# Kernel optimization log

Hardware: AMD Instinct MI355X
Metric: run time of the kernel (lower is better)

The kernel has to match this reference:

```python
import jax, jax.numpy as jnp
import numpy as np

# Static configuration (matches init_kwargs)
B, S = 1, 2048          # batch, stacked seq len
IN, D, OUT = 64, 1024, 128
H, HD = 16, 64          # heads, head_dim (rope over full head_dim)
L, FFN = 4, 4096        # layers, SwiGLU hidden
WIN = 128               # encoder_sliding_window
DOC = 256               # each of the 8 stacked documents has length 256
THETA = 10000.0
EPS = 1e-5


def setup_inputs() -> dict:
    key = jax.random.key(0)
    ks = jax.random.split(key, 12)
    std = 0.02  # init_base_std
    p = lambda k, shp: jax.random.normal(k, shp, jnp.float32) * std
    idx = jnp.arange(S, dtype=jnp.int32)
    return {
        "x": jax.random.normal(ks[0], (B, S, IN), jnp.float32),
        "emb_w": p(ks[1], (IN, D)),
        "emb_b": jnp.zeros((D,), jnp.float32),
        "wq": p(ks[2], (L, D, H * HD)),
        "wk": p(ks[3], (L, D, H * HD)),
        "wv": p(ks[4], (L, D, H * HD)),
        "wo": p(ks[5], (L, H * HD, D)),
        "attn_norm_w": jnp.ones((L, D), jnp.float32),
        "ffn_norm_w": jnp.ones((L, D), jnp.float32),
        "w1": p(ks[6], (L, D, FFN)),
        "w2": p(ks[7], (L, FFN, D)),
        "w3": p(ks[8], (L, D, FFN)),
        "out_norm_w": jnp.ones((D,), jnp.float32),
        "out_w": p(ks[9], (D, OUT)),
        "doc_id": idx // DOC,   # sequence-stacked document ids
        "tok_id": idx % DOC,    # per-document local token ids
    }


def _rmsnorm(x, w):
    return x * jax.lax.rsqrt(jnp.mean(x * x, axis=-1, keepdims=True) + EPS) * w


def _rope_cos_sin(tok_id):
    inv = 1.0 / (THETA ** (jnp.arange(0, HD, 2, dtype=jnp.float32) / HD))  # [HD/2]
    ang = tok_id.astype(jnp.float32)[:, None] * inv[None, :]               # [S, HD/2]
    return jnp.cos(ang), jnp.sin(ang)


def _apply_rope(x, cos, sin):
    # x: [B, S, H, HD]; rotate-half convention over head_dim
    x1, x2 = jnp.split(x, 2, axis=-1)
    c = cos[None, :, None, :]
    s = sin[None, :, None, :]
    return jnp.concatenate([x1 * c - x2 * s, x1 * s + x2 * c], axis=-1)


def reference(x, emb_w, emb_b, wq, wk, wv, wo, attn_norm_w, ffn_norm_w,
              w1, w2, w3, out_norm_w, out_w, doc_id, tok_id):
    # doc + sliding-window mask (the flex_attention mask_mod): same document
    same_doc = doc_id[:, None] == doc_id[None, :]
    t = tok_id.astype(jnp.int32)
    in_win = jnp.abs(t[:, None] - t[None, :]) < WIN
    mask = same_doc & in_win                       # [S, S] bool
    neg = jnp.asarray(jnp.finfo(jnp.float32).min, jnp.float32)

    cos, sin = _rope_cos_sin(tok_id)
    scale = 1.0 / np.sqrt(HD)

    h = x @ emb_w + emb_b                          # tok_embeddings: [B, S, D]

    def layer(h, p):
        wq_l, wk_l, wv_l, wo_l, anw, fnw, w1_l, w2_l, w3_l = p
        hn = _rmsnorm(h, anw)
        q = _apply_rope((hn @ wq_l).reshape(B, S, H, HD), cos, sin)
        k = _apply_rope((hn @ wk_l).reshape(B, S, H, HD), cos, sin)
        v = (hn @ wv_l).reshape(B, S, H, HD)
        scores = jnp.einsum("bqhd,bkhd->bhqk", q, k) * scale
        scores = jnp.where(mask[None, None], scores, neg)
        probs = jax.nn.softmax(scores, axis=-1)
        o = jnp.einsum("bhqk,bkhd->bqhd", probs, v).reshape(B, S, H * HD)
        h = h + o @ wo_l
        hn2 = _rmsnorm(h, fnw)
        ffn = (jax.nn.silu(hn2 @ w1_l) * (hn2 @ w3_l)) @ w2_l  # SwiGLU
        return h + ffn, None

    h, _ = jax.lax.scan(layer, h, (wq, wk, wv, wo, attn_norm_w, ffn_norm_w, w1, w2, w3))
    return _rmsnorm(h, out_norm_w) @ out_w         # output proj: [B, S, OUT]
```

## Files before the change

### kernel.cpp

```cpp
#include <hip/hip_runtime.h>
#include <hip/hip_bf16.h>

typedef __attribute__((ext_vector_type(8))) short short8;
typedef __attribute__((ext_vector_type(4))) float float4v;

__device__ __forceinline__ float bf2f(ushort u) {
    union { unsigned int i; float f; } x; x.i = ((unsigned int)u) << 16; return x.f;
}
__device__ __forceinline__ ushort f2bf(float f) {
    union { float f; unsigned int i; } x; x.f = f;
    unsigned int i = x.i;
    unsigned int r = (i + 0x7fffu + ((i >> 16) & 1u)) >> 16;
    return (ushort)r;
}

__global__ __launch_bounds__(256) void transpose4_f2b(const float* __restrict__ s0,
                                                      const float* __restrict__ s1,
                                                      const float* __restrict__ s2,
                                                      const float* __restrict__ s3,
                                                      ushort* __restrict__ dst,
                                                      int K, int N) {
    __shared__ ushort tile[64][68];
    const float* srcs[4] = {s0, s1, s2, s3};
    const float* src = srcs[blockIdx.z];
    ushort* d = dst + (size_t)blockIdx.z * K * N;
    const int t = threadIdx.x;
    const int n0 = blockIdx.x * 64, k0 = blockIdx.y * 64;
    const int tr = t >> 4, tc = (t & 15) * 4;
#pragma unroll
    for (int i = 0; i < 4; ++i) {
        int row = tr + i * 16;
        float4 v = *(const float4*)&src[(size_t)(k0 + row) * N + n0 + tc];
        tile[row][tc + 0] = f2bf(v.x);
        tile[row][tc + 1] = f2bf(v.y);
        tile[row][tc + 2] = f2bf(v.z);
        tile[row][tc + 3] = f2bf(v.w);
    }
    __syncthreads();
#pragma unroll
    for (int i = 0; i < 4; ++i) {
        int n = tr + i * 16;
        ushort4 v;
        v.x = tile[tc + 0][n]; v.y = tile[tc + 1][n];
        v.z = tile[tc + 2][n]; v.w = tile[tc + 3][n];
        *(ushort4*)&d[(size_t)(n0 + n) * K + k0 + tc] = v;
    }
}

__global__ __launch_bounds__(256) void embed_k(const float* __restrict__ x,
                                               const float* __restrict__ w,
                                               const float* __restrict__ b,
                                               float* __restrict__ h) {
    const int row = blockIdx.y;
    const int col = blockIdx.x * 256 + threadIdx.x;
    float acc = b[col];
#pragma unroll 8
    for (int k = 0; k < 64; ++k)
        acc += x[row * 64 + k] * w[k * 1024 + col];
    h[(size_t)row * 1024 + col] = acc;
}

__global__ __launch_bounds__(256) void rmsnorm_k(const float* __restrict__ h,
                                                 const float* __restrict__ w,
                                                 ushort* __restrict__ out) {
    const int row = blockIdx.x, t = threadIdx.x;
    float4 v = ((const float4*)(h + (size_t)row * 1024))[t];
    float ss = v.x * v.x + v.y * v.y + v.z * v.z + v.w * v.w;
#pragma unroll
    for (int off = 32; off > 0; off >>= 1) ss += __shfl_down(ss, off);
    __shared__ float red[4];
    if ((t & 63) == 0) red[t >> 6] = ss;
    __syncthreads();
    float inv = rsqrtf((red[0] + red[1] + red[2] + red[3]) * (1.0f / 1024.0f) + 1e-5f);
    float4 wv = ((const float4*)w)[t];
    ushort4 ov;
    ov.x = f2bf(v.x * inv * wv.x);
    ov.y = f2bf(v.y * inv * wv.y);
    ov.z = f2bf(v.z * inv * wv.z);
    ov.w = f2bf(v.w * inv * wv.w);
    *(ushort4*)&out[(size_t)row * 1024 + t * 4] = ov;
}

__global__ __launch_bounds__(256) void rope_table_k(float* __restrict__ ct,
                                                    float* __restrict__ st) {
    int idx = blockIdx.x * 256 + threadIdx.x;
    int s = idx >> 5, j = idx & 31;
    float inv = expf(-(float)j * (1.0f / 32.0f) * logf(10000.0f));
    float ang = (float)(s & 255) * inv;
    ct[idx] = cosf(ang);
    st[idx] = sinf(ang);
}

__global__ __launch_bounds__(256) void rope_apply_k(ushort* __restrict__ qkv,
                                                    const float* __restrict__ ct,
                                                    const float* __restrict__ st) {
    int idx = blockIdx.x * 256 + threadIdx.x;
    int j = idx & 31;
    int head = (idx >> 5) & 15;
    int s = idx >> 9;
    size_t base = (size_t)s * 3072 + head * 64 + j;
    float c = ct[s * 32 + j], sn = st[s * 32 + j];
    float x1 = bf2f(qkv[base]), x2 = bf2f(qkv[base + 32]);
    qkv[base] = f2bf(x1 * c - x2 * sn);
    qkv[base + 32] = f2bf(x1 * sn + x2 * c);
    x1 = bf2f(qkv[base + 1024]); x2 = bf2f(qkv[base + 1056]);
    qkv[base + 1024] = f2bf(x1 * c - x2 * sn);
    qkv[base + 1056] = f2bf(x1 * sn + x2 * c);
}

__global__ __launch_bounds__(256) void silu_mul_k(ushort* __restrict__ t13) {
    int idx = blockIdx.x * 256 + threadIdx.x;
    int s = idx >> 10, c4 = (idx & 1023) * 4;
    size_t b1 = (size_t)s * 8192 + c4;
    ushort4 a = *(ushort4*)&t13[b1];
    ushort4 b = *(ushort4*)&t13[b1 + 4096];
    float xs[4] = {bf2f(a.x), bf2f(a.y), bf2f(a.z), bf2f(a.w)};
    float ys[4] = {bf2f(b.x), bf2f(b.y), bf2f(b.z), bf2f(b.w)};
    ushort4 o;
    o.x = f2bf(xs[0] / (1.0f + __expf(-xs[0])) * ys[0]);
    o.y = f2bf(xs[1] / (1.0f + __expf(-xs[1])) * ys[1]);
    o.z = f2bf(xs[2] / (1.0f + __expf(-xs[2])) * ys[2]);
    o.w = f2bf(xs[3] / (1.0f + __expf(-xs[3])) * ys[3]);
    *(ushort4*)&t13[b1] = o;
}

__global__ __launch_bounds__(256) void reduce4_k(const ushort* __restrict__ p,
                                                 float* __restrict__ h,
                                                 int ldp, long zstr, int cbase) {
    const int s = blockIdx.x, c = threadIdx.x * 4;
    size_t base = (size_t)s * ldp + cbase + c;
    float a0 = 0, a1 = 0, a2 = 0, a3 = 0;
#pragma unroll
    for (int z = 0; z < 4; ++z) {
        ushort4 v = *(const ushort4*)&p[base + (size_t)z * zstr];
        a0 += bf2f(v.x); a1 += bf2f(v.y); a2 += bf2f(v.z); a3 += bf2f(v.w);
    }
    float4* hp = (float4*)&h[(size_t)s * 1024 + c];
    float4 cur = *hp;
    cur.x += a0; cur.y += a1; cur.z += a2; cur.w += a3;
    *hp = cur;
}

template <int OUT, int SK>
__global__ __launch_bounds__(256) void gemm_bt(const ushort* __restrict__ A, int lda,
                                               const ushort* __restrict__ Bt,
                                               void* __restrict__ Cp,
                                               int N, int K,
                                               int ldc, long zstr, int cbase) {
    __shared__ ushort As[128 * 32];
    __shared__ ushort Bs[128 * 32];
    const int tid = threadIdx.x, wave = tid >> 6, lane = tid & 63;
    const int quad = lane >> 4, l15 = lane & 15;
    const int m0 = blockIdx.y * 128, n0 = blockIdx.x * 128;
    const int wm = wave & 1, wn = wave >> 1;
    const int Kc = K / SK;
    const int kbeg = blockIdx.z * Kc, kend = kbeg + Kc;
    float4v acc[4][4] = {};
    for (int k0 = kbeg; k0 < kend; k0 += 32) {
        __syncthreads();
#pragma unroll
        for (int h = 0; h < 2; ++h) {
            int c = wave * 2 + h;
            int mrow = c * 16 + (lane >> 2);
            int kb = (lane & 3) * 16;
            const char* ga = (const char*)A + ((size_t)(m0 + mrow) * lda + k0) * 2 + kb;
            __builtin_amdgcn_global_load_lds(
                (const __attribute__((address_space(1))) void*)ga,
                (__attribute__((address_space(3))) void*)((char*)As + c * 1024), 16, 0, 0);
            const char* gb = (const char*)Bt + ((size_t)(n0 + mrow) * K + k0) * 2 + kb;
            __builtin_amdgcn_global_load_lds(
                (const __attribute__((address_space(1))) void*)gb,
                (__attribute__((address_space(3))) void*)((char*)Bs + c * 1024), 16, 0, 0);
        }
        __syncthreads();
        short8 af[4], bf[4];
#pragma unroll
        for (int i = 0; i < 4; ++i)
            af[i] = *(const short8*)((const char*)As + (wm * 64 + i * 16 + l15) * 64 + quad * 16);
#pragma unroll
        for (int j = 0; j < 4; ++j)
            bf[j] = *(const short8*)((const char*)Bs + (wn * 64 + j * 16 + l15) * 64 + quad * 16);
#pragma unroll
        for (int i = 0; i < 4; ++i)
#pragma unroll
            for (int j = 0; j < 4; ++j)
                acc[i][j] = __builtin_amdgcn_mfma_f32_16x16x32_bf16(af[i], bf[j], acc[i][j], 0, 0, 0);
    }
    const size_t zoff = (OUT == 3) ? (size_t)cbase + (size_t)blockIdx.z * zstr : 0;
#pragma unroll
    for (int i = 0; i < 4; ++i)
#pragma unroll
        for (int j = 0; j < 4; ++j)
#pragma unroll
            for (int r = 0; r < 4; ++r) {
                int row = m0 + wm * 64 + i * 16 + quad * 4 + r;
                int col = n0 + wn * 64 + j * 16 + l15;
                if (OUT == 0) {
                    ((ushort*)Cp)[(size_t)row * ldc + col] = f2bf(acc[i][j][r]);
                } else if (OUT == 2) {
                    ((float*)Cp)[(size_t)row * ldc + col] = acc[i][j][r];
                } else {
                    ((ushort*)Cp)[zoff + (size_t)row * ldc + col] = f2bf(acc[i][j][r]);
                }
            }
}

__global__ __launch_bounds__(512) void attention_k(const ushort* __restrict__ qkv,
                                                   ushort* __restrict__ o) {
    __shared__ ushort Vt[64 * 264];
    __shared__ ushort Pc[8][16 * 40];
    const int tid = threadIdx.x, wave = tid >> 6, lane = tid & 63;
    const int quad = lane >> 4, l15 = lane & 15;
    const int doc = blockIdx.x >> 5, head = (blockIdx.x >> 1) & 15, qh = blockIdx.x & 1;
    const size_t S0 = (size_t)doc * 256;

    const ushort* vb = qkv + 2048 + head * 64;
    for (int i = tid; i < 256 * 64; i += 512) {
        int key = i >> 6, d = i & 63;
        Vt[d * 264 + key] = vb[(S0 + key) * 3072 + d];
    }

    const int q0 = qh * 128 + wave * 16;
    const ushort* qbase = qkv + head * 64;
    const ushort* kbase = qkv + 1024 + head * 64;
    short8 af0 = *(const short8*)&qbase[(S0 + q0 + l15) * 3072 + quad * 8];
    short8 af1 = *(const short8*)&qbase[(S0 + q0 + l15) * 3072 + 32 + quad * 8];

    float4v acc[16];
#pragma unroll
    for (int nt = 0; nt < 16; ++nt) {
        short8 b0 = *(const short8*)&kbase[(S0 + nt * 16 + l15) * 3072 + quad * 8];
        short8 b1 = *(const short8*)&kbase[(S0 + nt * 16 + l15) * 3072 + 32 + quad * 8];
        float4v a = {0.0f, 0.0f, 0.0f, 0.0f};
        a = __builtin_amdgcn_mfma_f32_16x16x32_bf16(af0, b0, a, 0, 0, 0);
        a = __builtin_amdgcn_mfma_f32_16x16x32_bf16(af1, b1, a, 0, 0, 0);
        acc[nt] = a;
    }

    float mx[4] = {-1e30f, -1e30f, -1e30f, -1e30f};
#pragma unroll
    for (int nt = 0; nt < 16; ++nt)
#pragma unroll
        for (int r = 0; r < 4; ++r) {
            int qp = q0 + quad * 4 + r;
            int kp = nt * 16 + l15;
            int dlt = qp - kp;
            bool ok = (dlt < 128) && (dlt > -128);
            float s = ok ? acc[nt][r] * 0.125f : -1e30f;
            acc[nt][r] = s;
            mx[r] = fmaxf(mx[r], s);
        }
#pragma unroll
    for (int r = 0; r < 4; ++r) {
        mx[r] = fmaxf(mx[r], __shfl_xor(mx[r], 1));
        mx[r] = fmaxf(mx[r], __shfl_xor(mx[r], 2));
        mx[r] = fmaxf(mx[r], __shfl_xor(mx[r], 4));
        mx[r] = fmaxf(mx[r], __shfl_xor(mx[r], 8));
    }
    float sum[4] = {0.0f, 0.0f, 0.0f, 0.0f};
#pragma unroll
    for (int nt = 0; nt < 16; ++nt)
#pragma unroll
        for (int r = 0; r < 4; ++r) {
            float p = __expf(acc[nt][r] - mx[r]);
            acc[nt][r] = p;
            sum[r] += p;
        }
    float inv[4];
#pragma unroll
    for (int r = 0; r < 4; ++r) {
        sum[r] += __shfl_xor(sum[r], 1);
        sum[r] += __shfl_xor(sum[r], 2);
        sum[r] += __shfl_xor(sum[r], 4);
        sum[r] += __shfl_xor(sum[r], 8);
        inv[r] = 1.0f / sum[r];
    }

    __syncthreads();

    float4v oacc[4] = {};
    ushort* pcw = &Pc[wave][0];
#pragma unroll
    for (int ks = 0; ks < 8; ++ks) {
#pragma unroll
        for (int half = 0; half < 2; ++half) {
            int nt = ks * 2 + half;
#pragma unroll
            for (int r = 0; r < 4; ++r)
                pcw[(quad * 4 + r) * 40 + half * 16 + l15] = f2bf(acc[nt][r] * inv[r]);
        }
        __asm__ volatile("s_waitcnt lgkmcnt(0)" ::: "memory");
        short8 pf = *(const short8*)&pcw[l15 * 40 + quad * 8];
#pragma unroll
        for (int ntd = 0; ntd < 4; ++ntd) {
            short8 vf = *(const short8*)&Vt[(ntd * 16 + l15) * 264 + ks * 32 + quad * 8];
            oacc[ntd] = __builtin_amdgcn_mfma_f32_16x16x32_bf16(pf, vf, oacc[ntd], 0, 0, 0);
        }
    }
#pragma unroll
    for (int ntd = 0; ntd < 4; ++ntd)
#pragma unroll
        for (int r = 0; r < 4; ++r)
            o[(S0 + q0 + quad * 4 + r) * 1024 + head * 64 + ntd * 16 + l15] = f2bf(oacc[ntd][r]);
}

extern "C" void kernel_launch(void* const* d_in, const int* in_sizes, int n_in,
                              void* d_out, int out_size, void* d_ws, size_t ws_size,
                              hipStream_t stream) {
    const float* x     = (const float*)d_in[0];
    const float* emb_w = (const float*)d_in[1];
    const float* emb_b = (const float*)d_in[2];
    const float* wq    = (const float*)d_in[3];
    const float* wk    = (const float*)d_in[4];
    const float* wv    = (const float*)d_in[5];
    const float* wo    = (const float*)d_in[6];
    const float* anw   = (const float*)d_in[7];
    const float* fnw   = (const float*)d_in[8];
    const float* w1    = (const float*)d_in[9];
    const float* w2    = (const float*)d_in[10];
    const float* w3    = (const float*)d_in[11];
    const float* onw   = (const float*)d_in[12];
    const float* ow    = (const float*)d_in[13];

    char* ws = (char*)d_ws;
    float*  h    = (float*)(ws);
    ushort* hn   = (ushort*)(ws + (8u << 20));
    ushort* big  = (ushort*)(ws + (12u << 20));
    ushort* pwo  = (ushort*)(ws + (24u << 20));
    ushort* wbuf = (ushort*)(ws + (44u << 20));
    float*  cosT = (float*)(ws + (60u << 20));
    float*  sinT = (float*)(ws + (60u << 20) + (256u << 10));

    dim3 b256(256);
    rope_table_k<<<256, b256, 0, stream>>>(cosT, sinT);
    embed_k<<<dim3(4, 2048), b256, 0, stream>>>(x, emb_w, emb_b, h);

    for (int l = 0; l < 4; ++l) {
        const float* wq_l = wq + (size_t)l * 1024 * 1024;
        const float* wk_l = wk + (size_t)l * 1024 * 1024;
        const float* wv_l = wv + (size_t)l * 1024 * 1024;
        const float* wo_l = wo + (size_t)l * 1024 * 1024;
        const float* w1_l = w1 + (size_t)l * 1024 * 4096;
        const float* w2_l = w2 + (size_t)l * 4096 * 1024;
        const float* w3_l = w3 + (size_t)l * 1024 * 4096;

        transpose4_f2b<<<dim3(16, 16, 4), b256, 0, stream>>>(wq_l, wk_l, wv_l, wo_l,
                                                             wbuf, 1024, 1024);
        rmsnorm_k<<<2048, b256, 0, stream>>>(h, anw + (size_t)l * 1024, hn);
        gemm_bt<0, 1><<<dim3(24, 16), b256, 0, stream>>>(hn, 1024, wbuf, big,
                                                         3072, 1024, 3072, 0, 0);
        rope_apply_k<<<4096, b256, 0, stream>>>(big, cosT, sinT);
        attention_k<<<256, dim3(512), 0, stream>>>(big, hn);

        gemm_bt<3, 4><<<dim3(8, 16, 4), b256, 0, stream>>>(hn, 1024,
            wbuf + (size_t)3 * 1024 * 1024, pwo, 1024, 1024,
            1024, (long)2048 * 1024, 0);
        reduce4_k<<<2048, b256, 0, stream>>>(pwo, h, 1024, (long)2048 * 1024, 0);

        transpose4_f2b<<<dim3(64, 16, 2), b256, 0, stream>>>(w1_l, w3_l, w1_l, w1_l,
                                                             wbuf, 1024, 4096);
        rmsnorm_k<<<2048, b256, 0, stream>>>(h, fnw + (size_t)l * 1024, hn);
        gemm_bt<0, 1><<<dim3(64, 16), b256, 0, stream>>>(hn, 1024, wbuf, big,
                                                         8192, 1024, 8192, 0, 0);
        silu_mul_k<<<8192, b256, 0, stream>>>(big);

        transpose4_f2b<<<dim3(16, 64, 1), b256, 0, stream>>>(w2_l, w2_l, w2_l, w2_l,
                                                             wbuf, 4096, 1024);
        gemm_bt<3, 4><<<dim3(8, 16, 4), b256, 0, stream>>>(big, 8192, wbuf, big,
                                                           1024, 4096, 8192, 1024, 4096);
        reduce4_k<<<2048, b256, 0, stream>>>(big, h, 8192, 1024, 4096);
    }

    rmsnorm_k<<<2048, b256, 0, stream>>>(h, onw, hn);
    transpose4_f2b<<<dim3(2, 16, 1), b256, 0, stream>>>(ow, ow, ow, ow, wbuf, 1024, 128);
    gemm_bt<2, 1><<<dim3(1, 16), b256, 0, stream>>>(hn, 1024, wbuf, d_out,
                                                    128, 1024, 128, 0, 0);
}
```

Measured before the change: 1.071 ms.

## Fuse residual reduce with RMSNorm and SwiGLU into W1/W3 GEMM epilogue

```diff
diff --git a/kernel.cpp b/kernel.cpp
--- a/kernel.cpp
+++ b/kernel.cpp
@@ -79,6 +79,38 @@
     ov.z = f2bf(v.z * inv * wv.z);
     ov.w = f2bf(v.w * inv * wv.w);
     *(ushort4*)&out[(size_t)row * 1024 + t * 4] = ov;
+}
+
+__global__ __launch_bounds__(256) void reduce_rms_k(const ushort* __restrict__ p,
+                                                    float* __restrict__ h,
+                                                    const float* __restrict__ w,
+                                                    ushort* __restrict__ out) {
+    const int row = blockIdx.x, t = threadIdx.x;
+    const int c = t * 4;
+    size_t base = (size_t)row * 1024 + c;
+    float a0 = 0, a1 = 0, a2 = 0, a3 = 0;
+#pragma unroll
+    for (int z = 0; z < 4; ++z) {
+        ushort4 v = *(const ushort4*)&p[base + (size_t)z * 2048 * 1024];
+        a0 += bf2f(v.x); a1 += bf2f(v.y); a2 += bf2f(v.z); a3 += bf2f(v.w);
+    }
+    float4 cur = *(float4*)&h[base];
+    cur.x += a0; cur.y += a1; cur.z += a2; cur.w += a3;
+    *(float4*)&h[base] = cur;
+    float ss = cur.x * cur.x + cur.y * cur.y + cur.z * cur.z + cur.w * cur.w;
+#pragma unroll
+    for (int off = 32; off > 0; off >>= 1) ss += __shfl_down(ss, off);
+    __shared__ float red[4];
+    if ((t & 63) == 0) red[t >> 6] = ss;
+    __syncthreads();
+    float inv = rsqrtf((red[0] + red[1] + red[2] + red[3]) * (1.0f / 1024.0f) + 1e-5f);
+    float4 wv = ((const float4*)w)[t];
+    ushort4 ov;
+    ov.x = f2bf(cur.x * inv * wv.x);
+    ov.y = f2bf(cur.y * inv * wv.y);
+    ov.z = f2bf(cur.z * inv * wv.z);
+    ov.w = f2bf(cur.w * inv * wv.w);
+    *(ushort4*)&out[base] = ov;
 }
 
 __global__ __launch_bounds__(256) void rope_table_k(float* __restrict__ ct,
@@ -108,45 +140,12 @@
     qkv[base + 1056] = f2bf(x1 * sn + x2 * c);
 }
 
-__global__ __launch_bounds__(256) void silu_mul_k(ushort* __restrict__ t13) {
-    int idx = blockIdx.x * 256 + threadIdx.x;
-    int s = idx >> 10, c4 = (idx & 1023) * 4;
-    size_t b1 = (size_t)s * 8192 + c4;
-    ushort4 a = *(ushort4*)&t13[b1];
-    ushort4 b = *(ushort4*)&t13[b1 + 4096];
-    float xs[4] = {bf2f(a.x), bf2f(a.y), bf2f(a.z), bf2f(a.w)};
-    float ys[4] = {bf2f(b.x), bf2f(b.y), bf2f(b.z), bf2f(b.w)};
-    ushort4 o;
-    o.x = f2bf(xs[0] / (1.0f + __expf(-xs[0])) * ys[0]);
-    o.y = f2bf(xs[1] / (1.0f + __expf(-xs[1])) * ys[1]);
-    o.z = f2bf(xs[2] / (1.0f + __expf(-xs[2])) * ys[2]);
-    o.w = f2bf(xs[3] / (1.0f + __expf(-xs[3])) * ys[3]);
-    *(ushort4*)&t13[b1] = o;
-}
-
-__global__ __launch_bounds__(256) void reduce4_k(const ushort* __restrict__ p,
-                                                 float* __restrict__ h,
-                                                 int ldp, long zstr, int cbase) {
-    const int s = blockIdx.x, c = threadIdx.x * 4;
-    size_t base = (size_t)s * ldp + cbase + c;
-    float a0 = 0, a1 = 0, a2 = 0, a3 = 0;
-#pragma unroll
-    for (int z = 0; z < 4; ++z) {
-        ushort4 v = *(const ushort4*)&p[base + (size_t)z * zstr];
-        a0 += bf2f(v.x); a1 += bf2f(v.y); a2 += bf2f(v.z); a3 += bf2f(v.w);
-    }
-    float4* hp = (float4*)&h[(size_t)s * 1024 + c];
-    float4 cur = *hp;
-    cur.x += a0; cur.y += a1; cur.z += a2; cur.w += a3;
-    *hp = cur;
-}
-
 template <int OUT, int SK>
 __global__ __launch_bounds__(256) void gemm_bt(const ushort* __restrict__ A, int lda,
                                                const ushort* __restrict__ Bt,
                                                void* __restrict__ Cp,
                                                int N, int K,
-                                               int ldc, long zstr, int cbase) {
+                                               int ldc, long zstr) {
     __shared__ ushort As[128 * 32];
     __shared__ ushort Bs[128 * 32];
     const int tid = threadIdx.x, wave = tid >> 6, lane = tid & 63;
@@ -186,7 +185,7 @@
             for (int j = 0; j < 4; ++j)
                 acc[i][j] = __builtin_amdgcn_mfma_f32_16x16x32_bf16(af[i], bf[j], acc[i][j], 0, 0, 0);
     }
-    const size_t zoff = (OUT == 3) ? (size_t)cbase + (size_t)blockIdx.z * zstr : 0;
+    const size_t zoff = (OUT == 3) ? (size_t)blockIdx.z * zstr : 0;
 #pragma unroll
     for (int i = 0; i < 4; ++i)
 #pragma unroll
@@ -202,6 +201,70 @@
                 } else {
                     ((ushort*)Cp)[zoff + (size_t)row * ldc + col] = f2bf(acc[i][j][r]);
                 }
+            }
+}
+
+__global__ __launch_bounds__(256) void gemm_w13(const ushort* __restrict__ A,
+                                                const ushort* __restrict__ W,
+                                                ushort* __restrict__ G) {
+    __shared__ ushort As[128 * 32];
+    __shared__ ushort B1[128 * 32];
+    __shared__ ushort B3[128 * 32];
+    const int tid = threadIdx.x, wave = tid >> 6, lane = tid & 63;
+    const int quad = lane >> 4, l15 = lane & 15;
+    const int m0 = blockIdx.y * 128, n0 = blockIdx.x * 128;
+    const int wm = wave & 1, wn = wave >> 1;
+    float4v acc1[4][4] = {};
+    float4v acc3[4][4] = {};
+    for (int k0 = 0; k0 < 1024; k0 += 32) {
+        __syncthreads();
+#pragma unroll
+        for (int h = 0; h < 2; ++h) {
+            int c = wave * 2 + h;
+            int mrow = c * 16 + (lane >> 2);
+            int kb = (lane & 3) * 16;
+            const char* ga = (const char*)A + ((size_t)(m0 + mrow) * 1024 + k0) * 2 + kb;
+            __builtin_amdgcn_global_load_lds(
+                (const __attribute__((address_space(1))) void*)ga,
+                (__attribute__((address_space(3))) void*)((char*)As + c * 1024), 16, 0, 0);
+            const char* g1 = (const char*)W + ((size_t)(n0 + mrow) * 1024 + k0) * 2 + kb;
+            __builtin_amdgcn_global_load_lds(
+                (const __attribute__((address_space(1))) void*)g1,
+                (__attribute__((address_space(3))) void*)((char*)B1 + c * 1024), 16, 0, 0);
+            const char* g3 = (const char*)W + ((size_t)(4096 + n0 + mrow) * 1024 + k0) * 2 + kb;
+            __builtin_amdgcn_global_load_lds(
+                (const __attribute__((address_space(1))) void*)g3,
+                (__attribute__((address_space(3))) void*)((char*)B3 + c * 1024), 16, 0, 0);
+        }
+        __syncthreads();
+        short8 af[4], b1f[4], b3f[4];
+#pragma unroll
+        for (int i = 0; i < 4; ++i)
+            af[i] = *(const short8*)((const char*)As + (wm * 64 + i * 16 + l15) * 64 + quad * 16);
+#pragma unroll
+        for (int j = 0; j < 4; ++j) {
+            b1f[j] = *(const short8*)((const char*)B1 + (wn * 64 + j * 16 + l15) * 64 + quad * 16);
+            b3f[j] = *(const short8*)((const char*)B3 + (wn * 64 + j * 16 + l15) * 64 + quad * 16);
+        }
+#pragma unroll
+        for (int i = 0; i < 4; ++i)
+#pragma unroll
+            for (int j = 0; j < 4; ++j) {
+                acc1[i][j] = __builtin_amdgcn_mfma_f32_16x16x32_bf16(af[i], b1f[j], acc1[i][j], 0, 0, 0);
+                acc3[i][j] = __builtin_amdgcn_mfma_f32_16x16x32_bf16(af[i], b3f[j], acc3[i][j], 0, 0, 0);
+            }
+    }
+#pragma unroll
+    for (int i = 0; i < 4; ++i)
+#pragma unroll
+        for (int j = 0; j < 4; ++j)
+#pragma unroll
+            for (int r = 0; r < 4; ++r) {
+                int row = m0 + wm * 64 + i * 16 + quad * 4 + r;
+                int col = n0 + wn * 64 + j * 16 + l15;
+                float x = acc1[i][j][r], y = acc3[i][j][r];
+                float g = x / (1.0f + __expf(-x)) * y;
+                G[(size_t)row * 4096 + col] = f2bf(g);
             }
 }
 
@@ -326,14 +389,16 @@
     float*  h    = (float*)(ws);
     ushort* hn   = (ushort*)(ws + (8u << 20));
     ushort* big  = (ushort*)(ws + (12u << 20));
-    ushort* pwo  = (ushort*)(ws + (24u << 20));
+    ushort* pwo  = (ushort*)(ws + (28u << 20));
     ushort* wbuf = (ushort*)(ws + (44u << 20));
     float*  cosT = (float*)(ws + (60u << 20));
     float*  sinT = (float*)(ws + (60u << 20) + (256u << 10));
 
+    const long ZSTR = (long)2048 * 1024;
     dim3 b256(256);
     rope_table_k<<<256, b256, 0, stream>>>(cosT, sinT);
     embed_k<<<dim3(4, 2048), b256, 0, stream>>>(x, emb_w, emb_b, h);
+    rmsnorm_k<<<2048, b256, 0, stream>>>(h, anw, hn);
 
     for (int l = 0; l < 4; ++l) {
         const float* wq_l = wq + (size_t)l * 1024 * 1024;
@@ -346,33 +411,28 @@
 
         transpose4_f2b<<<dim3(16, 16, 4), b256, 0, stream>>>(wq_l, wk_l, wv_l, wo_l,
                                                              wbuf, 1024, 1024);
-        rmsnorm_k<<<2048, b256, 0, stream>>>(h, anw + (size_t)l * 1024, hn);
         gemm_bt<0, 1><<<dim3(24, 16), b256, 0, stream>>>(hn, 1024, wbuf, big,
-                                                         3072, 1024, 3072, 0, 0);
+                                                         3072, 1024, 3072, 0);
         rope_apply_k<<<4096, b256, 0, stream>>>(big, cosT, sinT);
         attention_k<<<256, dim3(512), 0, stream>>>(big, hn);
 
         gemm_bt<3, 4><<<dim3(8, 16, 4), b256, 0, stream>>>(hn, 1024,
-            wbuf + (size_t)3 * 1024 * 1024, pwo, 1024, 1024,
-            1024, (long)2048 * 1024, 0);
-        reduce4_k<<<2048, b256, 0, stream>>>(pwo, h, 1024, (long)2048 * 1024, 0);
+            wbuf + (size_t)3 * 1024 * 1024, pwo, 1024, 1024, 1024, ZSTR);
+        reduce_rms_k<<<2048, b256, 0, stream>>>(pwo, h, fnw + (size_t)l * 1024, hn);
 
         transpose4_f2b<<<dim3(64, 16, 2), b256, 0, stream>>>(w1_l, w3_l, w1_l, w1_l,
                                                              wbuf, 1024, 4096);
-        rmsnorm_k<<<2048, b256, 0, stream>>>(h, fnw + (size_t)l * 1024, hn);
-        gemm_bt<0, 1><<<dim3(64, 16), b256, 0, stream>>>(hn, 1024, wbuf, big,
-                                                         8192, 1024, 8192, 0, 0);
-        silu_mul_k<<<8192, b256, 0, stream>>>(big);
+        gemm_w13<<<dim3(32, 16), b256, 0, stream>>>(hn, wbuf, big);
 
         transpose4_f2b<<<dim3(16, 64, 1), b256, 0, stream>>>(w2_l, w2_l, w2_l, w2_l,
                                                              wbuf, 4096, 1024);
-        gemm_bt<3, 4><<<dim3(8, 16, 4), b256, 0, stream>>>(big, 8192, wbuf, big,
-                                                           1024, 4096, 8192, 1024, 4096);
-        reduce4_k<<<2048, b256, 0, stream>>>(big, h, 8192, 1024, 4096);
-    }
-
-    rmsnorm_k<<<2048, b256, 0, stream>>>(h, onw, hn);
+        gemm_bt<3, 4><<<dim3(8, 16, 4), b256, 0, stream>>>(big, 4096, wbuf, pwo,
+                                                           1024, 4096, 1024, ZSTR);
+        const float* nw = (l < 3) ? (anw + (size_t)(l + 1) * 1024) : onw;
+        reduce_rms_k<<<2048, b256, 0, stream>>>(pwo, h, nw, hn);
+    }
+
     transpose4_f2b<<<dim3(2, 16, 1), b256, 0, stream>>>(ow, ow, ow, ow, wbuf, 1024, 128);
     gemm_bt<2, 1><<<dim3(1, 16), b256, 0, stream>>>(hn, 1024, wbuf, d_out,
-                                                    128, 1024, 128, 0, 0);
-}
+                                                    128, 1024, 128, 0);
+}
```

Result: no change. 1.087 ms (+1.5%).
